# Performance work log

Measured on AMD Instinct MI355X. Metric: run time of the kernel, lower is better.

The kernel has to match this reference:

```python
import jax, jax.numpy as jnp
import numpy as np

T, N, F_IN, H1, H2, F_OUT = 48, 4096, 64, 64, 32, 64

def setup_inputs() -> dict:
    key = jax.random.key(0)
    ks = jax.random.split(key, 14)
    sc = 0.05
    x = jax.random.normal(ks[0], (T, N, F_IN), jnp.float32)
    adj = jax.random.uniform(ks[1], (N, N), jnp.float32) / N  # roughly row-normalized dense adjacency
    fc_w = jax.random.normal(ks[2], (F_IN, H1), jnp.float32) * sc
    fc_b = jnp.zeros((H1,), jnp.float32)
    Wz = jax.random.normal(ks[3], (H1, F_OUT), jnp.float32) * sc
    Wr = jax.random.normal(ks[4], (H1, F_OUT), jnp.float32) * sc
    Wh = jax.random.normal(ks[5], (H1, F_OUT), jnp.float32) * sc
    Lz = jax.random.normal(ks[6], (2 * F_OUT, F_OUT), jnp.float32) * sc
    Lr = jax.random.normal(ks[7], (2 * F_OUT, F_OUT), jnp.float32) * sc
    Lh = jax.random.normal(ks[8], (2 * F_OUT, F_OUT), jnp.float32) * sc
    bz = jnp.zeros((F_OUT,), jnp.float32)
    br = jnp.zeros((F_OUT,), jnp.float32)
    bh = jnp.zeros((F_OUT,), jnp.float32)
    return {"x": x, "adj": adj, "fc_w": fc_w, "fc_b": fc_b,
            "Wz": Wz, "Wr": Wr, "Wh": Wh,
            "Lz": Lz, "Lr": Lr, "Lh": Lh,
            "bz": bz, "br": br, "bh": bh}

def reference(x, adj, fc_w, fc_b, Wz, Wr, Wh, Lz, Lr, Lh, bz, br, bh):
    # relu(fc(x)) followed by relu(unsqueeze) == single relu
    xh = jax.nn.relu(x @ fc_w + fc_b)          # [T, N, H1]
    h0 = jnp.zeros((N, F_OUT), x.dtype)

    def step(h, xi):
        # TGCN cell: dense graph conv A @ (X W) feeding GRU-style gates
        az = adj @ (xi @ Wz)                   # [N, F_OUT]
        ar = adj @ (xi @ Wr)
        ah = adj @ (xi @ Wh)
        z = jax.nn.sigmoid(jnp.concatenate([az, h], axis=-1) @ Lz + bz)
        r = jax.nn.sigmoid(jnp.concatenate([ar, h], axis=-1) @ Lr + br)
        h_tilde = jnp.tanh(jnp.concatenate([ah, h * r], axis=-1) @ Lh + bh)
        h_new = z * h + (1.0 - z) * h_tilde
        return h_new, None

    h, _ = jax.lax.scan(step, h0, xh)
    return h[None]                              # [1, N, F_OUT]
```

## Files before the change

### kernel.cpp

```cpp
#include <hip/hip_runtime.h>

typedef unsigned short u16;
typedef unsigned char u8;
typedef short s16x8 __attribute__((ext_vector_type(8)));
typedef unsigned short u16x4 __attribute__((ext_vector_type(4)));
typedef float f32x4 __attribute__((ext_vector_type(4)));
typedef int i32x4 __attribute__((ext_vector_type(4)));
typedef int i32x8 __attribute__((ext_vector_type(8)));

#define AS1 __attribute__((address_space(1)))
#define AS3 __attribute__((address_space(3)))

__device__ __forceinline__ void g2l16(const void* g, void* l) {
  __builtin_amdgcn_global_load_lds((const AS1 void*)g, (AS3 void*)l, 16, 0, 0);
}

__device__ __forceinline__ float b2f(u16 u) {
  union { unsigned int i; float f; } x; x.i = ((unsigned int)u) << 16; return x.f;
}
__device__ __forceinline__ u16 f2b(float f) {
  unsigned int u = __builtin_bit_cast(unsigned int, f);
  return (u16)((u + 0x7fffu + ((u >> 16) & 1u)) >> 16);
}
__device__ __forceinline__ u8 f2e4m3(float v) {
  int p = __builtin_amdgcn_cvt_pk_fp8_f32(v, 0.f, 0, false);
  return (u8)(p & 0xff);
}
__device__ __forceinline__ float sigm(float x) { return 1.f / (1.f + __expf(-x)); }
__device__ __forceinline__ float tanh_f(float x) { return 2.f / (1.f + __expf(-2.f * x)) - 1.f; }


__global__ __launch_bounds__(256) void kpre(
    const float* __restrict__ a, u8* __restrict__ ab,
    const float* __restrict__ fcw, const float* __restrict__ fcb,
    const float* __restrict__ x, u8* __restrict__ xht,
    const float* __restrict__ Wz, const float* __restrict__ Wr, const float* __restrict__ Wh,
    const float* __restrict__ Lz, const float* __restrict__ Lr, const float* __restrict__ Lh,
    u16* __restrict__ wct, u16* __restrict__ lbt) {
  int b = blockIdx.x, tid = threadIdx.x;
  if (b < 4096) {
    size_t idx = (size_t)b * 256 + tid;
    const float4* src = (const float4*)a;
    unsigned int* dst = (unsigned int*)ab;
#pragma unroll
    for (int k = 0; k < 4; ++k) {
      float4 v = src[idx + (size_t)k * 1048576];
      unsigned int p = __builtin_amdgcn_cvt_pk_fp8_f32(v.x * 4096.f, v.y * 4096.f, 0, false);
      p = __builtin_amdgcn_cvt_pk_fp8_f32(v.z * 4096.f, v.w * 4096.f, p, true);
      dst[idx + (size_t)k * 1048576] = p;
    }
    return;
  }
  if (b < 4144) {
    int idx = (b - 4096) * 256 + tid;
    int c_cat = idx >> 6, hh = idx & 63;
    int g = c_cat >> 6, c = c_cat & 63;
    const float* W = (g == 0) ? Wz : (g == 1) ? Wr : Wh;
    const float* L = (g == 0) ? Lz : (g == 1) ? Lr : Lh;
    float acc = 0.f;
    for (int m = 0; m < 64; ++m) acc += W[hh * 64 + m] * L[m * 64 + c];
    wct[c_cat * 64 + hh] = f2b(acc);
    return;
  }
  if (b < 4147) {
    int g = b - 4144;
    const float* L = (g == 0) ? Lz : (g == 1) ? Lr : Lh;
    for (int i = 0; i < 16; ++i) {
      int idx = tid * 16 + i; int c = idx >> 6, hh = idx & 63;
      lbt[g * 4096 + c * 64 + hh] = f2b(L[(64 + hh) * 64 + c]);
    }
    return;
  }
  int kb = b - 4147;
  int t = kb >> 5, n0 = (kb & 31) * 128;
  __shared__ __align__(16) u16 xs[128 * 72];
  __shared__ __align__(16) u16 fw[64 * 72];
  __shared__ __align__(16) u8 xh8[64 * 128];
  __shared__ float fb[64];
  int w = tid >> 6, l = tid & 63;
#pragma unroll
  for (int i = 0; i < 16; ++i) {
    int idx = tid + i * 256;
    int h = idx & 63, f = idx >> 6;
    fw[h * 72 + f] = f2b(fcw[f * 64 + h]);
  }
  const float4* xg = (const float4*)(x + ((size_t)t * 4096 + n0) * 64);
#pragma unroll
  for (int i = 0; i < 8; ++i) {
    int f = tid + i * 256;
    float4 v = xg[f];
    u16x4 p; p[0] = f2b(v.x); p[1] = f2b(v.y); p[2] = f2b(v.z); p[3] = f2b(v.w);
    *(u16x4*)&xs[(f >> 4) * 72 + (f & 15) * 4] = p;
  }
  if (tid < 64) fb[tid] = fcb[tid];
  __syncthreads();

  int lm = l & 15, q = l >> 4;
  f32x4 acc[4][2];
#pragma unroll
  for (int i = 0; i < 4; ++i)
#pragma unroll
    for (int j = 0; j < 2; ++j)
#pragma unroll
      for (int r = 0; r < 4; ++r) acc[i][j][r] = 0.f;
#pragma unroll
  for (int s = 0; s < 2; ++s) {
    s16x8 af[4], bf[2];
#pragma unroll
    for (int i = 0; i < 4; ++i) af[i] = *(const s16x8*)&fw[(16 * i + lm) * 72 + 32 * s + q * 8];
#pragma unroll
    for (int j = 0; j < 2; ++j) bf[j] = *(const s16x8*)&xs[(32 * w + 16 * j + lm) * 72 + 32 * s + q * 8];
#pragma unroll
    for (int i = 0; i < 4; ++i)
#pragma unroll
      for (int j = 0; j < 2; ++j)
        acc[i][j] = __builtin_amdgcn_mfma_f32_16x16x32_bf16(af[i], bf[j], acc[i][j], 0, 0, 0);
  }
#pragma unroll
  for (int i = 0; i < 4; ++i)
#pragma unroll
    for (int j = 0; j < 2; ++j) {
      int node = 32 * w + 16 * j + lm;
      int h0 = 16 * i + q * 4;
#pragma unroll
      for (int r = 0; r < 4; ++r) {
        float v = acc[i][j][r] + fb[h0 + r];
        xh8[(h0 + r) * 128 + node] = f2e4m3(v > 0.f ? v : 0.f);
      }
    }
  __syncthreads();
  {
    int h = tid >> 2, seg = tid & 3;
    u8* dst = xht + (size_t)(t * 64 + h) * 4096 + n0 + seg * 32;
    const u8* src = &xh8[h * 128 + seg * 32];
    *(i32x4*)dst = *(const i32x4*)src;
    *(i32x4*)(dst + 16) = *(const i32x4*)(src + 16);
  }
}

__global__ __launch_bounds__(256) void k2(
    const u8* __restrict__ A, const u8* __restrict__ B, u16* __restrict__ M) {
  __shared__ __align__(16) u8 sh[81920];
  int tid = threadIdx.x, w = tid >> 6, l = tid & 63;
  int nt = blockIdx.x, mt = blockIdx.y;
  const u8* Ab = A + (size_t)mt * 128 * 4096;
  const u8* Bb = B + (size_t)nt * 192 * 4096;
  int lm = l & 15, q = l >> 4;
  int wm = w >> 1, wn = w & 1;
  int srow = l >> 3, scol = l & 7;
  f32x4 acc[4][6];
#pragma unroll
  for (int i = 0; i < 4; ++i)
#pragma unroll
    for (int j = 0; j < 6; ++j)
#pragma unroll
      for (int r = 0; r < 4; ++r) acc[i][j][r] = 0.f;

#define STAGE(bsel, kk)                                                       \
  do {                                                                        \
    u8* As_ = sh + (bsel) * 40960;                                            \
    u8* Bs_ = As_ + 16384;                                                    \
    _Pragma("unroll") for (int j = 0; j < 4; ++j) {      \
      int r0 = 32 * w + 8 * j;                                                \
      int row = r0 + srow;                                                    \
      int c = (scol - row) & 7;                                               \
      g2l16(Ab + (size_t)row * 4096 + (kk) + c * 16, As_ + r0 * 128);         \
    }                                                                         \
    _Pragma("unroll") for (int j = 0; j < 6; ++j) {      \
      int r0 = 48 * w + 8 * j;                                                \
      int row = r0 + srow;                                                    \
      int c = (scol - row) & 7;                                               \
      g2l16(Bb + (size_t)row * 4096 + (kk) + c * 16, Bs_ + r0 * 128);         \
    }                                                                         \
  } while (0)

  STAGE(0, 0);
  __syncthreads();

  for (int it = 0; it < 32; ++it) {
    int k0b = it * 128;
    int cur = it & 1;
    if (it < 31) STAGE(cur ^ 1, k0b + 128);
    const u8* As = sh + cur * 40960;
    const u8* Bs = As + 16384;
    i32x8 a8[4];
#pragma unroll
    for (int i = 0; i < 4; ++i) {
      int ra = 64 * wm + 16 * i + lm;
      int p0 = (2 * q + ra) & 7, p1 = (2 * q + 1 + ra) & 7;
      i32x4 lo = *(const i32x4*)&As[ra * 128 + p0 * 16];
      i32x4 hi = *(const i32x4*)&As[ra * 128 + p1 * 16];
      a8[i] = __builtin_shufflevector(lo, hi, 0, 1, 2, 3, 4, 5, 6, 7);
    }
#pragma unroll
    for (int j = 0; j < 6; ++j) {
      int rb = 96 * wn + 16 * j + lm;
      int q0 = (2 * q + rb) & 7, q1 = (2 * q + 1 + rb) & 7;
      i32x4 lo2 = *(const i32x4*)&Bs[rb * 128 + q0 * 16];
      i32x4 hi2 = *(const i32x4*)&Bs[rb * 128 + q1 * 16];
      i32x8 b8 = __builtin_shufflevector(lo2, hi2, 0, 1, 2, 3, 4, 5, 6, 7);
#pragma unroll
      for (int i = 0; i < 4; ++i)
        acc[i][j] = __builtin_amdgcn_mfma_scale_f32_16x16x128_f8f6f4(
            a8[i], b8, acc[i][j], 0, 0, 0, 127, 0, 127);
    }
    __syncthreads();
  }
#undef STAGE

  u16* tb = (u16*)sh;
  const float sc = 1.f / 4096.f;
#pragma unroll
  for (int p = 0; p < 2; ++p) {
    if (p) __syncthreads();
    if (wm == p) {
#pragma unroll
      for (int i = 0; i < 4; ++i)
#pragma unroll
        for (int j = 0; j < 6; ++j)
#pragma unroll
          for (int r = 0; r < 4; ++r)
            tb[(16 * i + 4 * q + r) * 200 + 96 * wn + 16 * j + lm] = f2b(acc[i][j][r] * sc);
    }
    __syncthreads();
    int row = tid >> 2, seg = tid & 3;
    u16* dst = M + (size_t)(mt * 128 + p * 64 + row) * 3072 + nt * 192 + seg * 48;
    const u16* src = &tb[row * 200 + seg * 48];
#pragma unroll
    for (int v = 0; v < 6; ++v)
      *(i32x4*)(dst + 8 * v) = *(const i32x4*)(src + 8 * v);
  }
}

__global__ __launch_bounds__(256) void k3(
    const u16* __restrict__ M, const u16* __restrict__ wct, const u16* __restrict__ lbt,
    const float* __restrict__ bz, const float* __restrict__ br, const float* __restrict__ bh,
    float* __restrict__ out) {
  __shared__ __align__(16) u16 hhi[1024], hlo[1024];
  __shared__ __align__(16) u16 rhi[1024], rlo[1024];
  int tid = threadIdx.x, w = tid >> 6, l = tid & 63;
  int nb0 = blockIdx.x * 16;
  int lm = l & 15, q = l >> 4;
  int am = lm & 7;
  int cb = 16 * w + q * 4;
  int rd0 = lm * 64 + ((q ^ am) * 8);
  int rd1 = lm * 64 + (((4 + q) ^ am) * 8);
  int wi  = lm * 64 + (((2 * w + (q >> 1)) ^ am) * 8) + 4 * (q & 1);
  s16x8 afw[3][2], afl[3][2];
#pragma unroll
  for (int g = 0; g < 3; ++g)
#pragma unroll
    for (int s = 0; s < 2; ++s) {
      afw[g][s] = *(const s16x8*)&wct[(size_t)(g * 64 + 16 * w + lm) * 64 + 32 * s + q * 8];
      afl[g][s] = *(const s16x8*)&lbt[(size_t)(g * 64 + 16 * w + lm) * 64 + 32 * s + q * 8];
    }
  for (int i = tid; i < 1024; i += 256) { hhi[i] = 0; hlo[i] = 0; }
  f32x4 bzv, brv, bhv, hv;
#pragma unroll
  for (int r = 0; r < 4; ++r) {
    bzv[r] = bz[cb + r]; brv[r] = br[cb + r]; bhv[r] = bh[cb + r]; hv[r] = 0.f;
  }
  const f32x4 zf = {0.f, 0.f, 0.f, 0.f};
  __syncthreads();

  const u16* Mrow = M + (size_t)(nb0 + lm) * 3072;
  s16x8 Mn[2];
  Mn[0] = *(const s16x8*)&Mrow[q * 8];
  Mn[1] = *(const s16x8*)&Mrow[32 + q * 8];
  f32x4 uzwC = __builtin_amdgcn_mfma_f32_16x16x32_bf16(afw[0][0], Mn[0], bzv, 0, 0, 0);
  uzwC = __builtin_amdgcn_mfma_f32_16x16x32_bf16(afw[0][1], Mn[1], uzwC, 0, 0, 0);
  f32x4 urwC = __builtin_amdgcn_mfma_f32_16x16x32_bf16(afw[1][0], Mn[0], brv, 0, 0, 0);
  urwC = __builtin_amdgcn_mfma_f32_16x16x32_bf16(afw[1][1], Mn[1], urwC, 0, 0, 0);
  f32x4 uhwC = __builtin_amdgcn_mfma_f32_16x16x32_bf16(afw[2][0], Mn[0], bhv, 0, 0, 0);
  uhwC = __builtin_amdgcn_mfma_f32_16x16x32_bf16(afw[2][1], Mn[1], uhwC, 0, 0, 0);

  for (int t = 0; t < 48; ++t) {
    if (t < 47) {
      Mn[0] = *(const s16x8*)&Mrow[(t + 1) * 64 + q * 8];
      Mn[1] = *(const s16x8*)&Mrow[(t + 1) * 64 + 32 + q * 8];
    }
    s16x8 hh0 = *(const s16x8*)&hhi[rd0], hh1 = *(const s16x8*)&hhi[rd1];
    s16x8 hl0 = *(const s16x8*)&hlo[rd0], hl1 = *(const s16x8*)&hlo[rd1];
    f32x4 uzA = __builtin_amdgcn_mfma_f32_16x16x32_bf16(afl[0][0], hh0, uzwC, 0, 0, 0);
    uzA = __builtin_amdgcn_mfma_f32_16x16x32_bf16(afl[0][1], hh1, uzA, 0, 0, 0);
    f32x4 uzB = __builtin_amdgcn_mfma_f32_16x16x32_bf16(afl[0][0], hl0, zf, 0, 0, 0);
    uzB = __builtin_amdgcn_mfma_f32_16x16x32_bf16(afl[0][1], hl1, uzB, 0, 0, 0);
    f32x4 urA = __builtin_amdgcn_mfma_f32_16x16x32_bf16(afl[1][0], hh0, urwC, 0, 0, 0);
    urA = __builtin_amdgcn_mfma_f32_16x16x32_bf16(afl[1][1], hh1, urA, 0, 0, 0);
    f32x4 urB = __builtin_amdgcn_mfma_f32_16x16x32_bf16(afl[1][0], hl0, zf, 0, 0, 0);
    urB = __builtin_amdgcn_mfma_f32_16x16x32_bf16(afl[1][1], hl1, urB, 0, 0, 0);
    f32x4 zv, rv;
#pragma unroll
    for (int r = 0; r < 4; ++r) {
      zv[r] = sigm(uzA[r] + uzB[r]);
      rv[r] = sigm(urA[r] + urB[r]);
    }
    {
      u16x4 phi, plo;
#pragma unroll
      for (int r = 0; r < 4; ++r) {
        float p = hv[r] * rv[r];
        u16 hi = f2b(p); phi[r] = hi; plo[r] = f2b(p - b2f(hi));
      }
      *(u16x4*)&rhi[wi] = phi;
      *(u16x4*)&rlo[wi] = plo;
    }
    __syncthreads();
    s16x8 rh0 = *(const s16x8*)&rhi[rd0], rh1 = *(const s16x8*)&rhi[rd1];
    s16x8 rl0 = *(const s16x8*)&rlo[rd0], rl1 = *(const s16x8*)&rlo[rd1];
    f32x4 uhA = __builtin_amdgcn_mfma_f32_16x16x32_bf16(afl[2][0], rh0, uhwC, 0, 0, 0);
    uhA = __builtin_amdgcn_mfma_f32_16x16x32_bf16(afl[2][1], rh1, uhA, 0, 0, 0);
    f32x4 uhB = __builtin_amdgcn_mfma_f32_16x16x32_bf16(afl[2][0], rl0, zf, 0, 0, 0);
    uhB = __builtin_amdgcn_mfma_f32_16x16x32_bf16(afl[2][1], rl1, uhB, 0, 0, 0);
    {
      u16x4 phi, plo;
#pragma unroll
      for (int r = 0; r < 4; ++r) {
        float th = tanh_f(uhA[r] + uhB[r]);
        float hn = zv[r] * hv[r] + (1.f - zv[r]) * th;
        hv[r] = hn;
        u16 hi = f2b(hn); phi[r] = hi; plo[r] = f2b(hn - b2f(hi));
      }
      *(u16x4*)&hhi[wi] = phi;
      *(u16x4*)&hlo[wi] = plo;
    }
    if (t < 47) {
      uzwC = __builtin_amdgcn_mfma_f32_16x16x32_bf16(afw[0][0], Mn[0], bzv, 0, 0, 0);
      uzwC = __builtin_amdgcn_mfma_f32_16x16x32_bf16(afw[0][1], Mn[1], uzwC, 0, 0, 0);
      urwC = __builtin_amdgcn_mfma_f32_16x16x32_bf16(afw[1][0], Mn[0], brv, 0, 0, 0);
      urwC = __builtin_amdgcn_mfma_f32_16x16x32_bf16(afw[1][1], Mn[1], urwC, 0, 0, 0);
      uhwC = __builtin_amdgcn_mfma_f32_16x16x32_bf16(afw[2][0], Mn[0], bhv, 0, 0, 0);
      uhwC = __builtin_amdgcn_mfma_f32_16x16x32_bf16(afw[2][1], Mn[1], uhwC, 0, 0, 0);
    }
    __syncthreads();
  }
#pragma unroll
  for (int r = 0; r < 4; ++r)
    out[(size_t)(nb0 + lm) * 64 + cb + r] = hv[r];
}

extern "C" void kernel_launch(void* const* d_in, const int* in_sizes, int n_in,
                              void* d_out, int out_size, void* d_ws, size_t ws_size,
                              hipStream_t stream) {
  const float* x   = (const float*)d_in[0];
  const float* adj = (const float*)d_in[1];
  const float* fcw = (const float*)d_in[2];
  const float* fcb = (const float*)d_in[3];
  const float* Wz  = (const float*)d_in[4];
  const float* Wr  = (const float*)d_in[5];
  const float* Wh  = (const float*)d_in[6];
  const float* Lz  = (const float*)d_in[7];
  const float* Lr  = (const float*)d_in[8];
  const float* Lh  = (const float*)d_in[9];
  const float* bz  = (const float*)d_in[10];
  const float* br  = (const float*)d_in[11];
  const float* bh  = (const float*)d_in[12];
  char* ws = (char*)d_ws;
  u8*  xht  = (u8*)(ws);
  u8*  adj8 = (u8*)(ws + (size_t)12582912);
  u16* Mm   = (u16*)(ws + (size_t)29360128);
  u16* wct  = (u16*)(ws + (size_t)54525952);
  u16* lbt  = (u16*)(ws + (size_t)54550528);
  float* outp = (float*)d_out;

  hipLaunchKernelGGL(kpre, dim3(5683), dim3(256), 0, stream,
                     adj, adj8, fcw, fcb, x, xht, Wz, Wr, Wh, Lz, Lr, Lh, wct, lbt);
  hipLaunchKernelGGL(k2, dim3(16, 32), dim3(256), 0, stream, adj8, xht, Mm);
  hipLaunchKernelGGL(k3, dim3(256), dim3(256), 0, stream, Mm, wct, lbt, bz, br, bh, outp);
}
```

Measured before the change: 256.4 us.

## Pre-tile FP8 adjacency into MFMA fragment layout and load A directly to registers

The adjacency quantization kernel now writes FP8 adj in a blocked layout matching the MFMA 16x16x128 A-fragment order. The GEMM kernel then loads each wave's A fragments straight from global memory as 32-byte vectors instead of staging them through LDS. This cuts LDS traffic and shared memory per block (80KB to 48KB), which may allow more blocks per CU. In exchange, the A loads are now synchronous global loads issued in the loop, so their latency is exposed unless the compiler overlaps them.

New measurement: 257.8 us. About the same (+0.6%).

```diff
diff --git a/kernel.cpp b/kernel.cpp
--- a/kernel.cpp
+++ b/kernel.cpp
@@ -44,10 +44,16 @@
     unsigned int* dst = (unsigned int*)ab;
 #pragma unroll
     for (int k = 0; k < 4; ++k) {
-      float4 v = src[idx + (size_t)k * 1048576];
+      size_t f = idx + (size_t)k * 1048576;
+      float4 v = src[f];
       unsigned int p = __builtin_amdgcn_cvt_pk_fp8_f32(v.x * 4096.f, v.y * 4096.f, 0, false);
       p = __builtin_amdgcn_cvt_pk_fp8_f32(v.z * 4096.f, v.w * 4096.f, p, true);
-      dst[idx + (size_t)k * 1048576] = p;
+      int row = (int)(f >> 10);
+      int col0 = ((int)f & 1023) << 2;
+      unsigned int dstb = (unsigned int)(((row >> 7) * 32 + (col0 >> 7)) << 14) +
+                          (((row >> 4) & 7) << 11) +
+                          (((row & 15) | (((col0 >> 5) & 3) << 4)) << 5) + (col0 & 31);
+      dst[dstb >> 2] = p;
     }
     return;
   }
@@ -140,14 +146,14 @@
 
 __global__ __launch_bounds__(256) void k2(
     const u8* __restrict__ A, const u8* __restrict__ B, u16* __restrict__ M) {
-  __shared__ __align__(16) u8 sh[81920];
+  __shared__ __align__(16) u8 sh[49152];
   int tid = threadIdx.x, w = tid >> 6, l = tid & 63;
   int nt = blockIdx.x, mt = blockIdx.y;
-  const u8* Ab = A + (size_t)mt * 128 * 4096;
   const u8* Bb = B + (size_t)nt * 192 * 4096;
   int lm = l & 15, q = l >> 4;
   int wm = w >> 1, wn = w & 1;
   int srow = l >> 3, scol = l & 7;
+  const u8* At = A + (size_t)mt * 32 * 16384 + (size_t)(4 * wm) * 2048 + (size_t)l * 32;
   f32x4 acc[4][6];
 #pragma unroll
   for (int i = 0; i < 4; ++i)
@@ -156,16 +162,9 @@
 #pragma unroll
       for (int r = 0; r < 4; ++r) acc[i][j][r] = 0.f;
 
-#define STAGE(bsel, kk)                                                       \
+#define STAGE_B(bsel, kk)                                                     \
   do {                                                                        \
-    u8* As_ = sh + (bsel) * 40960;                                            \
-    u8* Bs_ = As_ + 16384;                                                    \
-    _Pragma("unroll") for (int j = 0; j < 4; ++j) {      \
-      int r0 = 32 * w + 8 * j;                                                \
-      int row = r0 + srow;                                                    \
-      int c = (scol - row) & 7;                                               \
-      g2l16(Ab + (size_t)row * 4096 + (kk) + c * 16, As_ + r0 * 128);         \
-    }                                                                         \
+    u8* Bs_ = sh + (bsel) * 24576;                                            \
     _Pragma("unroll") for (int j = 0; j < 6; ++j) {      \
       int r0 = 48 * w + 8 * j;                                                \
       int row = r0 + srow;                                                    \
@@ -174,24 +173,17 @@
     }                                                                         \
   } while (0)
 
-  STAGE(0, 0);
+  STAGE_B(0, 0);
   __syncthreads();
 
   for (int it = 0; it < 32; ++it) {
-    int k0b = it * 128;
     int cur = it & 1;
-    if (it < 31) STAGE(cur ^ 1, k0b + 128);
-    const u8* As = sh + cur * 40960;
-    const u8* Bs = As + 16384;
     i32x8 a8[4];
 #pragma unroll
-    for (int i = 0; i < 4; ++i) {
-      int ra = 64 * wm + 16 * i + lm;
-      int p0 = (2 * q + ra) & 7, p1 = (2 * q + 1 + ra) & 7;
-      i32x4 lo = *(const i32x4*)&As[ra * 128 + p0 * 16];
-      i32x4 hi = *(const i32x4*)&As[ra * 128 + p1 * 16];
-      a8[i] = __builtin_shufflevector(lo, hi, 0, 1, 2, 3, 4, 5, 6, 7);
-    }
+    for (int i = 0; i < 4; ++i)
+      a8[i] = *(const i32x8*)(At + (size_t)it * 16384 + i * 2048);
+    if (it < 31) STAGE_B(cur ^ 1, (it + 1) * 128);
+    const u8* Bs = sh + cur * 24576;
 #pragma unroll
     for (int j = 0; j < 6; ++j) {
       int rb = 96 * wn + 16 * j + lm;
@@ -206,7 +198,7 @@
     }
     __syncthreads();
   }
-#undef STAGE
+#undef STAGE_B
 
   u16* tb = (u16*)sh;
   const float sc = 1.f / 4096.f;
```
